# Performance work log

Measured on AMD Instinct MI355X. Metric: run time of the kernel, lower is better.

The kernel has to match this reference:

```python
import jax, jax.numpy as jnp
import numpy as np

S, B, TD = 1024, 2, 138
D, H, Dh, L, F = 1024, 16, 64, 8, 2048
EPS = 1e-5


def setup_inputs() -> dict:
    key = jax.random.key(0)
    ks = jax.random.split(key, 32)
    std = 0.02

    def w(k, shape):
        return (jax.random.normal(k, shape, jnp.float32) * std)

    return {
        'tokens': jax.random.normal(ks[0], (S, B, TD), jnp.float32),
        'Win': w(ks[1], (D, TD)), 'bin_': jnp.zeros((D,), jnp.float32),
        'pos_emb': w(ks[2], (S, D)),
        'Wq': w(ks[3], (L, D, D)), 'bq': jnp.zeros((L, D), jnp.float32),
        'Wk': w(ks[4], (L, D, D)), 'bk': jnp.zeros((L, D), jnp.float32),
        'Wv': w(ks[5], (L, D, D)), 'bv': jnp.zeros((L, D), jnp.float32),
        'Wo': w(ks[6], (L, D, D)), 'bo': jnp.zeros((L, D), jnp.float32),
        'W1': w(ks[7], (L, F, D)), 'b1': jnp.zeros((L, F), jnp.float32),
        'W2': w(ks[8], (L, D, F)), 'b2': jnp.zeros((L, D), jnp.float32),
        'g1': jnp.ones((L, D), jnp.float32), 'be1': jnp.zeros((L, D), jnp.float32),
        'g2': jnp.ones((L, D), jnp.float32), 'be2': jnp.zeros((L, D), jnp.float32),
        'Wh': w(ks[9], (1, D)), 'bh': jnp.zeros((1,), jnp.float32),
    }


def _ln(x, g, b):
    mu = jnp.mean(x, axis=-1, keepdims=True)
    var = jnp.mean(jnp.square(x - mu), axis=-1, keepdims=True)
    return (x - mu) * jax.lax.rsqrt(var + EPS) * g + b


def _rope_tables(seq_len):
    inv_freq = 1.0 / (10000.0 ** (jnp.arange(0, Dh, 2, dtype=jnp.float32) / Dh))
    ang = jnp.arange(seq_len, dtype=jnp.float32)[:, None] * inv_freq  # (S, Dh/2)
    cos = jnp.repeat(jnp.cos(ang), 2, axis=-1)  # (S, Dh) interleaved
    sin = jnp.repeat(jnp.sin(ang), 2, axis=-1)
    return cos, sin


def _apply_rope(x, cos, sin):
    # x: (B, H, S, Dh); rotate_every_two: pairs (x0, x1) -> (-x1, x0)
    rot = jnp.stack([-x[..., 1::2], x[..., 0::2]], axis=-1).reshape(x.shape)
    return x * cos + rot * sin


def reference(tokens, Win, bin_, pos_emb, Wq, bq, Wk, bk, Wv, bv, Wo, bo,
              W1, b1, W2, b2, g1, be1, g2, be2, Wh, bh):
    s = tokens.shape[0]
    x = jnp.einsum('sbt,dt->sbd', tokens, Win) + bin_ + pos_emb[:s, None, :]
    cos, sin = _rope_tables(s)
    causal = jnp.tril(jnp.ones((s, s), dtype=bool))
    scale = 1.0 / np.sqrt(Dh)

    def to_heads(y):  # (S,B,D) -> (B,H,S,Dh)
        return jnp.transpose(y.reshape(s, -1, H, Dh), (1, 2, 0, 3))

    def layer(x, p):
        wq, bq_, wk, bk_, wv, bv_, wo, bo_, w1, b1_, w2, b2_, g1_, be1_, g2_, be2_ = p
        qh = _apply_rope(to_heads(jnp.einsum('sbd,ed->sbe', x, wq) + bq_), cos, sin)
        kh = _apply_rope(to_heads(jnp.einsum('sbd,ed->sbe', x, wk) + bk_), cos, sin)
        vh = to_heads(jnp.einsum('sbd,ed->sbe', x, wv) + bv_)
        scores = jnp.einsum('bhqd,bhkd->bhqk', qh, kh) * scale
        scores = jnp.where(causal, scores, -jnp.inf)
        attn = jax.nn.softmax(scores, axis=-1)
        o = jnp.einsum('bhqk,bhkd->bhqd', attn, vh)  # (B,H,S,Dh)
        o = jnp.transpose(o, (2, 0, 1, 3)).reshape(s, -1, D)
        attn_out = jnp.einsum('sbd,ed->sbe', o, wo) + bo_
        src2 = _ln(x + attn_out, g1_, be1_)
        ff = jnp.einsum('sbf,df->sbd', jax.nn.relu(jnp.einsum('sbd,fd->sbf', src2, w1) + b1_), w2) + b2_
        return _ln(src2 + ff, g2_, be2_), None

    params = (Wq, bq, Wk, bk, Wv, bv, Wo, bo, W1, b1, W2, b2, g1, be1, g2, be2)
    x, _ = jax.lax.scan(layer, x, params)
    return jnp.einsum('sbd,od->sbo', x, Wh) + bh  # (S, B, 1)
```

## Files before the change

### kernel.cpp

```cpp
#include <hip/hip_runtime.h>
#include <hip/hip_bf16.h>

typedef __hip_bfloat16 bf16;
typedef float f32x4 __attribute__((ext_vector_type(4)));
typedef float f32x16 __attribute__((ext_vector_type(16)));
typedef short s16x8 __attribute__((ext_vector_type(8)));
typedef int i32x4 __attribute__((ext_vector_type(4)));

#define S_LEN 1024
#define BATCH 2
#define TDIM 138
#define KPAD 160
#define DMOD 1024
#define NHEAD 16
#define DHEAD 64
#define NLAYER 8
#define FDIM 2048
#define MROWS 2048
static const size_t DD_ = (size_t)DMOD * DMOD;
static const size_t FD_ = (size_t)FDIM * DMOD;

__device__ __forceinline__ void load_lds16(const bf16* g, bf16* l) {
  __builtin_amdgcn_global_load_lds((const __attribute__((address_space(1))) void*)g,
                                   (__attribute__((address_space(3))) void*)l, 16, 0, 0);
}

__device__ __forceinline__ unsigned pack2(float a, float b) {
  unsigned x = __builtin_bit_cast(unsigned short, __float2bfloat16(a));
  unsigned y = __builtin_bit_cast(unsigned short, __float2bfloat16(b));
  return x | (y << 16);
}

__device__ __forceinline__ int chunk_start(int c) {
  return c == 0 ? 0 : (c == 1 ? 32 : (c == 2 ? 56 : 72));
}

__global__ __launch_bounds__(256) void f2b_layer(
    const float4* __restrict__ Wq, const float4* __restrict__ Wk,
    const float4* __restrict__ Wv, const float4* __restrict__ Wo,
    const float4* __restrict__ W1, const float4* __restrict__ W2,
    ushort4* __restrict__ dst) {
  int i = blockIdx.x * 256 + threadIdx.x;
  const int DD4 = (int)(DD_ / 4), FD4 = (int)(FD_ / 4);
  if (i >= 4 * DD4 + 2 * FD4) return;
  const float4* src; int off;
  if (i < 3 * DD4) { int w = i / DD4; off = i - w * DD4; src = w == 0 ? Wq : (w == 1 ? Wk : Wv); }
  else if (i < 4 * DD4) { src = Wo; off = i - 3 * DD4; }
  else if (i < 4 * DD4 + FD4) { src = W1; off = i - 4 * DD4; }
  else { src = W2; off = i - 4 * DD4 - FD4; }
  float4 v = src[off];
  ushort4 o;
  o.x = __builtin_bit_cast(unsigned short, __float2bfloat16(v.x));
  o.y = __builtin_bit_cast(unsigned short, __float2bfloat16(v.y));
  o.z = __builtin_bit_cast(unsigned short, __float2bfloat16(v.z));
  o.w = __builtin_bit_cast(unsigned short, __float2bfloat16(v.w));
  dst[i] = o;
}

__global__ __launch_bounds__(256) void pad_cvt(const float* __restrict__ in,
                                               bf16* __restrict__ out, int R) {
  int i = blockIdx.x * 256 + threadIdx.x;
  if (i >= R * KPAD) return;
  int r = i / KPAD, t = i - r * KPAD;
  out[i] = __float2bfloat16(t < TDIM ? in[r * TDIM + t] : 0.0f);
}

__global__ __launch_bounds__(256) void rope_table(float2* __restrict__ t) {
  int idx = blockIdx.x * 256 + threadIdx.x;
  if (idx >= S_LEN * 32) return;
  int s = idx >> 5, i = idx & 31;
  float freq = __expf(-(float)i * (2.0f / (float)DHEAD) * 9.210340371976184f);
  float sn, cs;
  sincosf((float)s * freq, &sn, &cs);
  t[idx] = make_float2(cs, sn);
}

template<int EPI, int SPLITK>
__global__ __launch_bounds__(256) void gemm64(
    const bf16* __restrict__ A, const bf16* __restrict__ W,
    const float* __restrict__ b0p, const float* __restrict__ b1p, const float* __restrict__ b2p,
    const float2* __restrict__ rope2, float* __restrict__ Cf,
    bf16* __restrict__ Cb0, bf16* __restrict__ Cb1, bf16* __restrict__ Cb2,
    int N, int K, int nby) {
  constexpr int ASZ = 64 * 32, BSZ = 128 * 32;
  __shared__ bf16 As[2 * ASZ];
  __shared__ bf16 Bs[2 * BSZ];
  int nwg = gridDim.x, bid = blockIdx.x;
  int wg = (bid & 7) * (nwg >> 3) + (bid >> 3);
  int nbx = N >> 7;
  int by = wg % nby, bx2 = wg / nby;
  int kh = 0, bx = bx2;
  if constexpr (SPLITK == 2) { bx = bx2 % nbx; kh = bx2 / nbx; }
  int bn = bx * 128, bm = by * 64;
  int Kh = K / SPLITK, koff = kh * Kh;
  int tid = threadIdx.x, lane = tid & 63, w = tid >> 6;
  int lo = lane & 15, hi = lane >> 4;
  int wr = (w >> 1) * 32, wc = (w & 1) * 64;
  f32x4 acc[2][4] = {};

  int srow = tid >> 2, sseg = (tid & 3) * 8;
  const bf16* gA = A + (size_t)(bm + srow) * K + koff + sseg;
  const bf16* gB = W + (size_t)(bn + srow) * K + koff + sseg;
  bf16* lA = As + srow * 32 + sseg;
  bf16* lB = Bs + srow * 32 + sseg;

  auto STAGE = [&](int k0, int b) {
    load_lds16(gA + k0, lA + b * ASZ);
    load_lds16(gB + k0, lB + b * BSZ);
    load_lds16(gB + (size_t)64 * K + k0, lB + b * BSZ + 64 * 32);
  };

  int nt = Kh / 32;
  STAGE(0, 0);
  __syncthreads();
  int cur = 0;
  for (int t = 0; t < nt; t++) {
    if (t + 1 < nt) STAGE((t + 1) * 32, cur ^ 1);
    const bf16* Ab = As + cur * ASZ;
    const bf16* Bb = Bs + cur * BSZ;
    s16x8 af[2], bfr[4];
#pragma unroll
    for (int mi = 0; mi < 2; mi++) af[mi] = *(const s16x8*)(Ab + (wr + mi * 16 + lo) * 32 + hi * 8);
#pragma unroll
    for (int nj = 0; nj < 4; nj++) bfr[nj] = *(const s16x8*)(Bb + (wc + nj * 16 + lo) * 32 + hi * 8);
#pragma unroll
    for (int mi = 0; mi < 2; mi++)
#pragma unroll
      for (int nj = 0; nj < 4; nj++)
        acc[mi][nj] = __builtin_amdgcn_mfma_f32_16x16x32_bf16(af[mi], bfr[nj], acc[mi][nj], 0, 0, 0);
    __syncthreads();
    cur ^= 1;
  }

#pragma unroll
  for (int mi = 0; mi < 2; mi++)
#pragma unroll
    for (int nj = 0; nj < 4; nj++)
#pragma unroll
      for (int r = 0; r < 4; r++) {
        int m = bm + wr + mi * 16 + hi * 4 + r;
        int n = bn + wc + nj * 16 + lo;
        float v = acc[mi][nj][r];
        if constexpr (EPI == 0) {
          int which = n >> 10;
          int d = n & 1023, h = d >> 6, dh = d & 63;
          int s = m >> 1, bb = m & 1;
          const float* bp = which == 0 ? b0p : (which == 1 ? b1p : b2p);
          v += bp[d];
          if (which < 2) {
            float pv = __shfl_xor(v, 1);
            float2 cn = rope2[s * 32 + (dh >> 1)];
            float o = (dh & 1) ? (v * cn.x + pv * cn.y) : (v * cn.x - pv * cn.y);
            bf16* dst = which == 0 ? Cb0 : Cb1;
            dst[(((size_t)(bb * NHEAD + h)) * S_LEN + s) * DHEAD + dh] = __float2bfloat16(o);
          } else {
            Cb2[(((size_t)(bb * NHEAD + h)) * DHEAD + dh) * S_LEN + s] = __float2bfloat16(v);
          }
        } else if constexpr (EPI == 1) {
          if (SPLITK == 1 || kh == 0) v += b0p[n];
          Cf[((size_t)kh * MROWS + m) * N + n] = v;
        } else if constexpr (EPI == 2) {
          Cb0[(size_t)m * N + n] = __float2bfloat16(fmaxf(v + b0p[n], 0.0f));
        } else {
          float v2 = v + b0p[n] + b1p[(size_t)(m >> 1) * DMOD + n];
          Cf[(size_t)m * N + n] = v2;
          Cb0[(size_t)m * N + n] = __float2bfloat16(v2);
        }
      }
}

__global__ __launch_bounds__(256) void flash_part(const bf16* __restrict__ Q,
    const bf16* __restrict__ K, const bf16* __restrict__ Vt,
    float* __restrict__ pO, float* __restrict__ pML) {
  int bid = blockIdx.x;
  int xcd = bid & 7, idx = bid >> 3;
  int bh = xcd * 4 + idx / 20;
  int w = threadIdx.x >> 6, lane = threadIdx.x & 63;
  int widx = (idx % 20) * 4 + w;
  int c = widx < 32 ? 0 : (widx < 56 ? 1 : (widx < 72 ? 2 : 3));
  int qt = widx - chunk_start(c) + 8 * c;
  int l31 = lane & 31, hi1 = lane >> 5;
  int q0 = qt * 32, kc0 = c * 256;
  int kend = min(kc0 + 256, q0 + 32);
  int nkt = (kend - kc0 + 31) >> 5;

  const size_t qkb = (size_t)bh * S_LEN * DHEAD;
  const bf16* qp = Q + qkb + (size_t)(q0 + l31) * DHEAD + hi1 * 8;
  s16x8 bq0 = *(const s16x8*)(qp);
  s16x8 bq1 = *(const s16x8*)(qp + 16);
  s16x8 bq2 = *(const s16x8*)(qp + 32);
  s16x8 bq3 = *(const s16x8*)(qp + 48);
  const bf16* kB = K + qkb;
  const bf16* vB = Vt + qkb;
  f32x16 accO0 = {}, accO1 = {};
  float mv = -INFINITY, lv = 0.0f;
  const float SC = 0.18033688011112042f;

  auto loadTile = [&](int kc, s16x8& k0, s16x8& k1, s16x8& k2, s16x8& k3,
                      s16x8& v0, s16x8& v1, s16x8& v2, s16x8& v3) {
    const bf16* kp = kB + (size_t)(kc + l31) * DHEAD + hi1 * 8;
    k0 = *(const s16x8*)(kp);
    k1 = *(const s16x8*)(kp + 16);
    k2 = *(const s16x8*)(kp + 32);
    k3 = *(const s16x8*)(kp + 48);
    const bf16* vp = vB + (size_t)l31 * S_LEN + kc + hi1 * 8;
    v0 = *(const s16x8*)(vp);
    v1 = *(const s16x8*)(vp + 16);
    v2 = *(const s16x8*)(vp + (size_t)32 * S_LEN);
    v3 = *(const s16x8*)(vp + (size_t)32 * S_LEN + 16);
  };

  auto computeTile = [&](int kc, s16x8 ka0, s16x8 ka1, s16x8 ka2, s16x8 ka3,
                         s16x8 va00, s16x8 va01, s16x8 va10, s16x8 va11) {
    f32x16 st = {};
    st = __builtin_amdgcn_mfma_f32_32x32x16_bf16(ka0, bq0, st, 0, 0, 0);
    st = __builtin_amdgcn_mfma_f32_32x32x16_bf16(ka1, bq1, st, 0, 0, 0);
    st = __builtin_amdgcn_mfma_f32_32x32x16_bf16(ka2, bq2, st, 0, 0, 0);
    st = __builtin_amdgcn_mfma_f32_32x32x16_bf16(ka3, bq3, st, 0, 0, 0);

    bool diag = (kc >= q0);
    float pmax = -INFINITY;
#pragma unroll
    for (int j = 0; j < 16; j++) {
      float s = st[j] * SC;
      if (diag) {
        int krow = kc + (j & 3) + 8 * (j >> 2) + 4 * hi1;
        if (krow > q0 + l31) s = -INFINITY;
      }
      st[j] = s;
      pmax = fmaxf(pmax, s);
    }
    pmax = fmaxf(pmax, __shfl_xor(pmax, 32));
    float mnew = fmaxf(mv, pmax);
    float fs = exp2f(mv - mnew);
    float sum = 0.0f;
#pragma unroll
    for (int j = 0; j < 16; j++) {
      float e = exp2f(st[j] - mnew);
      st[j] = e;
      sum += e;
    }
    sum += __shfl_xor(sum, 32);
    lv = lv * fs + sum;
    mv = mnew;
    accO0 = accO0 * fs;
    accO1 = accO1 * fs;

    unsigned w0 = pack2(st[0], st[1]),   w1 = pack2(st[2], st[3]);
    unsigned w2 = pack2(st[4], st[5]),   w3 = pack2(st[6], st[7]);
    unsigned w4 = pack2(st[8], st[9]),   w5 = pack2(st[10], st[11]);
    unsigned w6 = pack2(st[12], st[13]), w7 = pack2(st[14], st[15]);
    unsigned xw0 = (unsigned)__shfl_xor((int)w0, 32), xw1 = (unsigned)__shfl_xor((int)w1, 32);
    unsigned xw2 = (unsigned)__shfl_xor((int)w2, 32), xw3 = (unsigned)__shfl_xor((int)w3, 32);
    unsigned xw4 = (unsigned)__shfl_xor((int)w4, 32), xw5 = (unsigned)__shfl_xor((int)w5, 32);
    unsigned xw6 = (unsigned)__shfl_xor((int)w6, 32), xw7 = (unsigned)__shfl_xor((int)w7, 32);
    bool hb = (hi1 != 0);
    i32x4 f0, f1;
    f0.x = (int)(hb ? xw2 : w0); f0.y = (int)(hb ? xw3 : w1);
    f0.z = (int)(hb ? w2 : xw0); f0.w = (int)(hb ? w3 : xw1);
    f1.x = (int)(hb ? xw6 : w4); f1.y = (int)(hb ? xw7 : w5);
    f1.z = (int)(hb ? w6 : xw4); f1.w = (int)(hb ? w7 : xw5);
    s16x8 pf0 = __builtin_bit_cast(s16x8, f0);
    s16x8 pf1 = __builtin_bit_cast(s16x8, f1);
    accO0 = __builtin_amdgcn_mfma_f32_32x32x16_bf16(va00, pf0, accO0, 0, 0, 0);
    accO0 = __builtin_amdgcn_mfma_f32_32x32x16_bf16(va01, pf1, accO0, 0, 0, 0);
    accO1 = __builtin_amdgcn_mfma_f32_32x32x16_bf16(va10, pf0, accO1, 0, 0, 0);
    accO1 = __builtin_amdgcn_mfma_f32_32x32x16_bf16(va11, pf1, accO1, 0, 0, 0);
  };

  s16x8 A0, A1, A2, A3, A4, A5, A6, A7;
  s16x8 B0, B1, B2, B3, B4, B5, B6, B7;
  loadTile(kc0, A0, A1, A2, A3, A4, A5, A6, A7);
  for (int kt = 0; kt < nkt; kt += 2) {
    if (kt + 1 < nkt) loadTile(kc0 + (kt + 1) * 32, B0, B1, B2, B3, B4, B5, B6, B7);
    computeTile(kc0 + kt * 32, A0, A1, A2, A3, A4, A5, A6, A7);
    if (kt + 1 < nkt) {
      if (kt + 2 < nkt) loadTile(kc0 + (kt + 2) * 32, A0, A1, A2, A3, A4, A5, A6, A7);
      computeTile(kc0 + (kt + 1) * 32, B0, B1, B2, B3, B4, B5, B6, B7);
    }
  }

  int pbase = bh * 80 + widx;
  float* po = pO + (size_t)pbase * 2048 + l31 * 64 + 4 * hi1;
#pragma unroll
  for (int jj = 0; jj < 4; jj++) {
    f32x4 v0 = {accO0[4 * jj], accO0[4 * jj + 1], accO0[4 * jj + 2], accO0[4 * jj + 3]};
    f32x4 v1 = {accO1[4 * jj], accO1[4 * jj + 1], accO1[4 * jj + 2], accO1[4 * jj + 3]};
    *(f32x4*)(po + 8 * jj) = v0;
    *(f32x4*)(po + 32 + 8 * jj) = v1;
  }
  if (hi1 == 0) {
    pML[pbase * 64 + l31] = mv;
    pML[pbase * 64 + 32 + l31] = lv;
  }
}

__global__ __launch_bounds__(256) void flash_merge(const float* __restrict__ pO,
    const float* __restrict__ pML, bf16* __restrict__ O) {
  int bid = blockIdx.x;
  int xcd = bid & 7, idx = bid >> 3;
  int bh = xcd * 4 + idx / 32, qt = idx % 32;
  int b = bh >> 4, h = bh & 15;
  int nch = (qt >> 3) + 1;
  int t = threadIdx.x;
  int dh = t & 63, r0 = t >> 6;
  int ibase = bh * 80;
#pragma unroll
  for (int j = 0; j < 8; j++) {
    int row = j * 4 + r0;
    float ms = -INFINITY;
    for (int cc = 0; cc < nch; cc++) {
      int wi = chunk_start(cc) + qt - 8 * cc;
      ms = fmaxf(ms, pML[(ibase + wi) * 64 + row]);
    }
    float l = 0.0f, o = 0.0f;
    for (int cc = 0; cc < nch; cc++) {
      int wi = chunk_start(cc) + qt - 8 * cc;
      float wgt = exp2f(pML[(ibase + wi) * 64 + row] - ms);
      l += wgt * pML[(ibase + wi) * 64 + 32 + row];
      o += wgt * pO[(size_t)(ibase + wi) * 2048 + row * 64 + dh];
    }
    int q = qt * 32 + row;
    O[((size_t)q * BATCH + b) * DMOD + h * DHEAD + dh] = __float2bfloat16(o / l);
  }
}

__global__ __launch_bounds__(256) void ln_kernel(const float* __restrict__ a,
    const float* __restrict__ r0, const float* __restrict__ r1,
    const float* __restrict__ g, const float* __restrict__ be,
    float* __restrict__ outf, bf16* __restrict__ outb) {
  int m = blockIdx.x;
  int tid = threadIdx.x;
  float vals[4];
  float s1 = 0.f, s2 = 0.f;
  for (int j = 0; j < 4; j++) {
    int d = tid + j * 256;
    size_t i = (size_t)m * DMOD + d;
    float v = a[i] + r0[i] + r1[i];
    vals[j] = v; s1 += v; s2 += v * v;
  }
  __shared__ float red[8];
  for (int d = 1; d < 64; d <<= 1) { s1 += __shfl_xor(s1, d); s2 += __shfl_xor(s2, d); }
  int w = tid >> 6, lane = tid & 63;
  if (lane == 0) { red[w] = s1; red[4 + w] = s2; }
  __syncthreads();
  s1 = red[0] + red[1] + red[2] + red[3];
  s2 = red[4] + red[5] + red[6] + red[7];
  float mean = s1 * (1.0f / DMOD);
  float var = s2 * (1.0f / DMOD) - mean * mean;
  float rstd = rsqrtf(var + 1e-5f);
  for (int j = 0; j < 4; j++) {
    int d = tid + j * 256;
    float o = (vals[j] - mean) * rstd * g[d] + be[d];
    outf[(size_t)m * DMOD + d] = o;
    outb[(size_t)m * DMOD + d] = __float2bfloat16(o);
  }
}

__global__ __launch_bounds__(256) void head_kernel(const float* __restrict__ x,
    const float* __restrict__ Wh, const float* __restrict__ bh, float* __restrict__ out) {
  int m = blockIdx.x * 4 + (threadIdx.x >> 6);
  int lane = threadIdx.x & 63;
  float s = 0.f;
  for (int j = 0; j < 16; j++) {
    int d = lane + j * 64;
    s += x[(size_t)m * DMOD + d] * Wh[d];
  }
  for (int d = 1; d < 64; d <<= 1) s += __shfl_xor(s, d);
  if (lane == 0) out[m] = s + bh[0];
}

extern "C" void kernel_launch(void* const* d_in, const int* in_sizes, int n_in,
                              void* d_out, int out_size, void* d_ws, size_t ws_size,
                              hipStream_t stream) {
  (void)in_sizes; (void)n_in; (void)out_size; (void)ws_size;
  const float* tokens = (const float*)d_in[0];
  const float* Win    = (const float*)d_in[1];
  const float* binp   = (const float*)d_in[2];
  const float* pos    = (const float*)d_in[3];
  const float* Wq     = (const float*)d_in[4];
  const float* bq     = (const float*)d_in[5];
  const float* Wk     = (const float*)d_in[6];
  const float* bk     = (const float*)d_in[7];
  const float* Wv     = (const float*)d_in[8];
  const float* bv     = (const float*)d_in[9];
  const float* Wo     = (const float*)d_in[10];
  const float* bo     = (const float*)d_in[11];
  const float* W1     = (const float*)d_in[12];
  const float* b1     = (const float*)d_in[13];
  const float* W2     = (const float*)d_in[14];
  const float* b2     = (const float*)d_in[15];
  const float* g1     = (const float*)d_in[16];
  const float* be1    = (const float*)d_in[17];
  const float* g2     = (const float*)d_in[18];
  const float* be2    = (const float*)d_in[19];
  const float* Wh     = (const float*)d_in[20];
  const float* bhp    = (const float*)d_in[21];
  float* out = (float*)d_out;

  char* p = (char*)d_ws;
  auto alloc = [&](size_t bytes) { char* r = p; p += (bytes + 255) & ~(size_t)255; return r; };
  float* xf   = (float*)alloc((size_t)MROWS * DMOD * 4);
  bf16*  xb   = (bf16*) alloc((size_t)MROWS * DMOD * 2);
  float* x2f  = (float*)alloc((size_t)MROWS * DMOD * 4);
  bf16*  x2b  = (bf16*) alloc((size_t)MROWS * DMOD * 2);
  float* tmpf = (float*)alloc((size_t)2 * MROWS * DMOD * 4);
  bf16*  qb   = (bf16*) alloc((size_t)MROWS * DMOD * 2);
  bf16*  kb   = (bf16*) alloc((size_t)MROWS * DMOD * 2);
  bf16*  vt   = (bf16*) alloc((size_t)MROWS * DMOD * 2);
  bf16*  ob   = (bf16*) alloc((size_t)MROWS * DMOD * 2);
  bf16*  hb   = (bf16*) alloc((size_t)MROWS * FDIM * 2);
  bf16*  wb   = (bf16*) alloc((4 * DD_ + 2 * FD_) * 2);
  bf16*  tokb = (bf16*) alloc((size_t)MROWS * KPAD * 2);
  bf16*  winb = (bf16*) alloc((size_t)DMOD * KPAD * 2);
  float2* rope2 = (float2*)alloc((size_t)S_LEN * 32 * 8);
  float* pO   = (float*)alloc((size_t)32 * 80 * 2048 * 4);
  float* pML  = (float*)alloc((size_t)32 * 80 * 64 * 4);

  rope_table<<<(S_LEN * 32 + 255) / 256, 256, 0, stream>>>(rope2);
  pad_cvt<<<(MROWS * KPAD + 255) / 256, 256, 0, stream>>>(tokens, tokb, MROWS);
  pad_cvt<<<(DMOD * KPAD + 255) / 256, 256, 0, stream>>>(Win, winb, DMOD);
  gemm64<3, 1><<<256, 256, 0, stream>>>(
      tokb, winb, binp, pos, nullptr, nullptr,
      xf, xb, nullptr, nullptr, DMOD, KPAD, 32);

  const int nW4 = (int)((4 * DD_ + 2 * FD_) / 4);

  for (int l = 0; l < NLAYER; l++) {
    f2b_layer<<<(nW4 + 255) / 256, 256, 0, stream>>>(
        (const float4*)(Wq + l * DD_), (const float4*)(Wk + l * DD_),
        (const float4*)(Wv + l * DD_), (const float4*)(Wo + l * DD_),
        (const float4*)(W1 + l * FD_), (const float4*)(W2 + l * FD_), (ushort4*)wb);

    gemm64<0, 1><<<768, 256, 0, stream>>>(
        xb, wb, bq + l * DMOD, bk + l * DMOD, bv + l * DMOD, rope2,
        nullptr, qb, kb, vt, 3 * DMOD, DMOD, 32);

    flash_part<<<640, 256, 0, stream>>>(qb, kb, vt, pO, pML);
    flash_merge<<<1024, 256, 0, stream>>>(pO, pML, ob);

    gemm64<1, 2><<<512, 256, 0, stream>>>(
        ob, wb + 3 * DD_, bo + l * DMOD, nullptr, nullptr, nullptr,
        tmpf, nullptr, nullptr, nullptr, DMOD, DMOD, 32);

    ln_kernel<<<MROWS, 256, 0, stream>>>(xf, tmpf, tmpf + (size_t)MROWS * DMOD,
                                         g1 + l * DMOD, be1 + l * DMOD, x2f, x2b);

    gemm64<2, 1><<<512, 256, 0, stream>>>(
        x2b, wb + 4 * DD_, b1 + l * FDIM, nullptr, nullptr, nullptr,
        nullptr, hb, nullptr, nullptr, FDIM, DMOD, 32);

    gemm64<1, 2><<<512, 256, 0, stream>>>(
        hb, wb + 4 * DD_ + FD_, b2 + l * DMOD, nullptr, nullptr, nullptr,
        tmpf, nullptr, nullptr, nullptr, DMOD, FDIM, 32);

    ln_kernel<<<MROWS, 256, 0, stream>>>(x2f, tmpf, tmpf + (size_t)MROWS * DMOD,
                                         g2 + l * DMOD, be2 + l * DMOD, xf, xb);
  }

  head_kernel<<<MROWS / 4, 256, 0, stream>>>(xf, Wh, bhp, out);
}
```

Measured before the change: 1.457 ms.

## Deepen GEMM K-tile to 64 with XOR-swizzled LDS and batch weight conversion

The GEMM now stages 64-wide K tiles instead of 32, halving the number of barrier-separated iterations. It applies an XOR swizzle to the LDS column layout to avoid bank conflicts on the 128-byte row stride. KPAD is raised to 192 so the input projection's K divides by 64. All 8 layers' fp32 weights are converted to bf16 in one up-front grid-stride kernel when workspace allows, replacing the per-layer conversion launches. The larger tiles double LDS usage per block, which may reduce occupancy.

```diff
diff --git a/kernel.cpp b/kernel.cpp
--- a/kernel.cpp
+++ b/kernel.cpp
@@ -10,7 +10,7 @@
 #define S_LEN 1024
 #define BATCH 2
 #define TDIM 138
-#define KPAD 160
+#define KPAD 192
 #define DMOD 1024
 #define NHEAD 16
 #define DHEAD 64
@@ -19,6 +19,7 @@
 #define MROWS 2048
 static const size_t DD_ = (size_t)DMOD * DMOD;
 static const size_t FD_ = (size_t)FDIM * DMOD;
+static const size_t LW_ = 4 * DD_ + 2 * FD_;
 
 __device__ __forceinline__ void load_lds16(const bf16* g, bf16* l) {
   __builtin_amdgcn_global_load_lds((const __attribute__((address_space(1))) void*)g,
@@ -35,26 +36,30 @@
   return c == 0 ? 0 : (c == 1 ? 32 : (c == 2 ? 56 : 72));
 }
 
-__global__ __launch_bounds__(256) void f2b_layer(
+__global__ __launch_bounds__(256) void f2b_all(
     const float4* __restrict__ Wq, const float4* __restrict__ Wk,
     const float4* __restrict__ Wv, const float4* __restrict__ Wo,
     const float4* __restrict__ W1, const float4* __restrict__ W2,
-    ushort4* __restrict__ dst) {
-  int i = blockIdx.x * 256 + threadIdx.x;
-  const int DD4 = (int)(DD_ / 4), FD4 = (int)(FD_ / 4);
-  if (i >= 4 * DD4 + 2 * FD4) return;
-  const float4* src; int off;
-  if (i < 3 * DD4) { int w = i / DD4; off = i - w * DD4; src = w == 0 ? Wq : (w == 1 ? Wk : Wv); }
-  else if (i < 4 * DD4) { src = Wo; off = i - 3 * DD4; }
-  else if (i < 4 * DD4 + FD4) { src = W1; off = i - 4 * DD4; }
-  else { src = W2; off = i - 4 * DD4 - FD4; }
-  float4 v = src[off];
-  ushort4 o;
-  o.x = __builtin_bit_cast(unsigned short, __float2bfloat16(v.x));
-  o.y = __builtin_bit_cast(unsigned short, __float2bfloat16(v.y));
-  o.z = __builtin_bit_cast(unsigned short, __float2bfloat16(v.z));
-  o.w = __builtin_bit_cast(unsigned short, __float2bfloat16(v.w));
-  dst[i] = o;
+    ushort4* __restrict__ dst, int nlay) {
+  const int DD4 = (int)(DD_ / 4), FD4 = (int)(FD_ / 4), LW4 = 4 * DD4 + 2 * FD4;
+  int total = nlay * LW4;
+  for (int i = blockIdx.x * 256 + threadIdx.x; i < total; i += gridDim.x * 256) {
+    int l = i / LW4, off = i - l * LW4;
+    const float4* src; int o2;
+    if (off < 3 * DD4) {
+      int w = off / DD4; o2 = off - w * DD4 + l * DD4;
+      src = w == 0 ? Wq : (w == 1 ? Wk : Wv);
+    } else if (off < 4 * DD4) { src = Wo; o2 = off - 3 * DD4 + l * DD4; }
+    else if (off < 4 * DD4 + FD4) { src = W1; o2 = off - 4 * DD4 + l * FD4; }
+    else { src = W2; o2 = off - 4 * DD4 - FD4 + l * FD4; }
+    float4 v = src[o2];
+    ushort4 o;
+    o.x = __builtin_bit_cast(unsigned short, __float2bfloat16(v.x));
+    o.y = __builtin_bit_cast(unsigned short, __float2bfloat16(v.y));
+    o.z = __builtin_bit_cast(unsigned short, __float2bfloat16(v.z));
+    o.w = __builtin_bit_cast(unsigned short, __float2bfloat16(v.w));
+    dst[i] = o;
+  }
 }
 
 __global__ __launch_bounds__(256) void pad_cvt(const float* __restrict__ in,
@@ -82,7 +87,7 @@
     const float2* __restrict__ rope2, float* __restrict__ Cf,
     bf16* __restrict__ Cb0, bf16* __restrict__ Cb1, bf16* __restrict__ Cb2,
     int N, int K, int nby) {
-  constexpr int ASZ = 64 * 32, BSZ = 128 * 32;
+  constexpr int ASZ = 64 * 64, BSZ = 128 * 64;
   __shared__ bf16 As[2 * ASZ];
   __shared__ bf16 Bs[2 * BSZ];
   int nwg = gridDim.x, bid = blockIdx.x;
@@ -98,36 +103,46 @@
   int wr = (w >> 1) * 32, wc = (w & 1) * 64;
   f32x4 acc[2][4] = {};
 
-  int srow = tid >> 2, sseg = (tid & 3) * 8;
-  const bf16* gA = A + (size_t)(bm + srow) * K + koff + sseg;
-  const bf16* gB = W + (size_t)(bn + srow) * K + koff + sseg;
-  bf16* lA = As + srow * 32 + sseg;
-  bf16* lB = Bs + srow * 32 + sseg;
+  int srow = tid >> 3;
+  int scol = (tid & 7) * 8;
+  int scolsw = scol ^ ((srow & 7) << 3);
+  const bf16* gA = A + (size_t)(bm + srow) * K + koff + scolsw;
+  const bf16* gB = W + (size_t)(bn + srow) * K + koff + scolsw;
+  bf16* lA = As + srow * 64 + scol;
+  bf16* lB = Bs + srow * 64 + scol;
 
   auto STAGE = [&](int k0, int b) {
     load_lds16(gA + k0, lA + b * ASZ);
+    load_lds16(gA + (size_t)32 * K + k0, lA + b * ASZ + 32 * 64);
     load_lds16(gB + k0, lB + b * BSZ);
-    load_lds16(gB + (size_t)64 * K + k0, lB + b * BSZ + 64 * 32);
+    load_lds16(gB + (size_t)32 * K + k0, lB + b * BSZ + 32 * 64);
+    load_lds16(gB + (size_t)64 * K + k0, lB + b * BSZ + 64 * 64);
+    load_lds16(gB + (size_t)96 * K + k0, lB + b * BSZ + 96 * 64);
   };
 
-  int nt = Kh / 32;
+  int nt = Kh / 64;
   STAGE(0, 0);
   __syncthreads();
   int cur = 0;
+  int rsw = (lo & 7) << 3;
   for (int t = 0; t < nt; t++) {
-    if (t + 1 < nt) STAGE((t + 1) * 32, cur ^ 1);
+    if (t + 1 < nt) STAGE((t + 1) * 64, cur ^ 1);
     const bf16* Ab = As + cur * ASZ;
     const bf16* Bb = Bs + cur * BSZ;
-    s16x8 af[2], bfr[4];
-#pragma unroll
-    for (int mi = 0; mi < 2; mi++) af[mi] = *(const s16x8*)(Ab + (wr + mi * 16 + lo) * 32 + hi * 8);
-#pragma unroll
-    for (int nj = 0; nj < 4; nj++) bfr[nj] = *(const s16x8*)(Bb + (wc + nj * 16 + lo) * 32 + hi * 8);
-#pragma unroll
-    for (int mi = 0; mi < 2; mi++)
-#pragma unroll
-      for (int nj = 0; nj < 4; nj++)
-        acc[mi][nj] = __builtin_amdgcn_mfma_f32_16x16x32_bf16(af[mi], bfr[nj], acc[mi][nj], 0, 0, 0);
+#pragma unroll
+    for (int ks = 0; ks < 2; ks++) {
+      int col = ((ks * 32 + hi * 8) ^ rsw);
+      s16x8 af[2], bfr[4];
+#pragma unroll
+      for (int mi = 0; mi < 2; mi++) af[mi] = *(const s16x8*)(Ab + (wr + mi * 16 + lo) * 64 + col);
+#pragma unroll
+      for (int nj = 0; nj < 4; nj++) bfr[nj] = *(const s16x8*)(Bb + (wc + nj * 16 + lo) * 64 + col);
+#pragma unroll
+      for (int mi = 0; mi < 2; mi++)
+#pragma unroll
+        for (int nj = 0; nj < 4; nj++)
+          acc[mi][nj] = __builtin_amdgcn_mfma_f32_16x16x32_bf16(af[mi], bfr[nj], acc[mi][nj], 0, 0, 0);
+    }
     __syncthreads();
     cur ^= 1;
   }
@@ -373,7 +388,7 @@
 extern "C" void kernel_launch(void* const* d_in, const int* in_sizes, int n_in,
                               void* d_out, int out_size, void* d_ws, size_t ws_size,
                               hipStream_t stream) {
-  (void)in_sizes; (void)n_in; (void)out_size; (void)ws_size;
+  (void)in_sizes; (void)n_in; (void)out_size;
   const float* tokens = (const float*)d_in[0];
   const float* Win    = (const float*)d_in[1];
   const float* binp   = (const float*)d_in[2];
@@ -410,48 +425,59 @@
   bf16*  vt   = (bf16*) alloc((size_t)MROWS * DMOD * 2);
   bf16*  ob   = (bf16*) alloc((size_t)MROWS * DMOD * 2);
   bf16*  hb   = (bf16*) alloc((size_t)MROWS * FDIM * 2);
-  bf16*  wb   = (bf16*) alloc((4 * DD_ + 2 * FD_) * 2);
   bf16*  tokb = (bf16*) alloc((size_t)MROWS * KPAD * 2);
   bf16*  winb = (bf16*) alloc((size_t)DMOD * KPAD * 2);
   float2* rope2 = (float2*)alloc((size_t)S_LEN * 32 * 8);
   float* pO   = (float*)alloc((size_t)32 * 80 * 2048 * 4);
   float* pML  = (float*)alloc((size_t)32 * 80 * 64 * 4);
 
+  size_t used = (size_t)(p - (char*)d_ws);
+  bool big = (ws_size - used) >= (size_t)NLAYER * LW_ * 2 + 1024;
+  int nlayConv = big ? NLAYER : 1;
+  bf16* wb = (bf16*)alloc((size_t)nlayConv * LW_ * 2);
+
   rope_table<<<(S_LEN * 32 + 255) / 256, 256, 0, stream>>>(rope2);
   pad_cvt<<<(MROWS * KPAD + 255) / 256, 256, 0, stream>>>(tokens, tokb, MROWS);
   pad_cvt<<<(DMOD * KPAD + 255) / 256, 256, 0, stream>>>(Win, winb, DMOD);
+  if (big)
+    f2b_all<<<2048, 256, 0, stream>>>(
+        (const float4*)Wq, (const float4*)Wk, (const float4*)Wv,
+        (const float4*)Wo, (const float4*)W1, (const float4*)W2,
+        (ushort4*)wb, NLAYER);
+
   gemm64<3, 1><<<256, 256, 0, stream>>>(
       tokb, winb, binp, pos, nullptr, nullptr,
       xf, xb, nullptr, nullptr, DMOD, KPAD, 32);
 
-  const int nW4 = (int)((4 * DD_ + 2 * FD_) / 4);
-
   for (int l = 0; l < NLAYER; l++) {
-    f2b_layer<<<(nW4 + 255) / 256, 256, 0, stream>>>(
-        (const float4*)(Wq + l * DD_), (const float4*)(Wk + l * DD_),
-        (const float4*)(Wv + l * DD_), (const float4*)(Wo + l * DD_),
-        (const float4*)(W1 + l * FD_), (const float4*)(W2 + l * FD_), (ushort4*)wb);
+    if (!big)
+      f2b_all<<<2048, 256, 0, stream>>>(
+          (const float4*)(Wq + l * DD_), (const float4*)(Wk + l * DD_),
+          (const float4*)(Wv + l * DD_), (const float4*)(Wo + l * DD_),
+          (const float4*)(W1 + l * FD_), (const float4*)(W2 + l * FD_),
+          (ushort4*)wb, 1);
+    bf16* wbl = big ? wb + (size_t)l * LW_ : wb;
 
     gemm64<0, 1><<<768, 256, 0, stream>>>(
-        xb, wb, bq + l * DMOD, bk + l * DMOD, bv + l * DMOD, rope2,
+        xb, wbl, bq + l * DMOD, bk + l * DMOD, bv + l * DMOD, rope2,
         nullptr, qb, kb, vt, 3 * DMOD, DMOD, 32);
 
     flash_part<<<640, 256, 0, stream>>>(qb, kb, vt, pO, pML);
     flash_merge<<<1024, 256, 0, stream>>>(pO, pML, ob);
 
     gemm64<1, 2><<<512, 256, 0, stream>>>(
-        ob, wb + 3 * DD_, bo + l * DMOD, nullptr, nullptr, nullptr,
+        ob, wbl + 3 * DD_, bo + l * DMOD, nullptr, nullptr, nullptr,
         tmpf, nullptr, nullptr, nullptr, DMOD, DMOD, 32);
 
     ln_kernel<<<MROWS, 256, 0, stream>>>(xf, tmpf, tmpf + (size_t)MROWS * DMOD,
                                          g1 + l * DMOD, be1 + l * DMOD, x2f, x2b);
 
     gemm64<2, 1><<<512, 256, 0, stream>>>(
-        x2b, wb + 4 * DD_, b1 + l * FDIM, nullptr, nullptr, nullptr,
+        x2b, wbl + 4 * DD_, b1 + l * FDIM, nullptr, nullptr, nullptr,
         nullptr, hb, nullptr, nullptr, FDIM, DMOD, 32);
 
     gemm64<1, 2><<<512, 256, 0, stream>>>(
-        hb, wb + 4 * DD_ + FD_, b2 + l * DMOD, nullptr, nullptr, nullptr,
+        hb, wbl + 4 * DD_ + FD_, b2 + l * DMOD, nullptr, nullptr, nullptr,
         tmpf, nullptr, nullptr, nullptr, DMOD, FDIM, 32);
 
     ln_kernel<<<MROWS, 256, 0, stream>>>(x2f, tmpf, tmpf + (size_t)MROWS * DMOD,
```

Measured after the change: 1.452 ms. Within noise of the previous version (-0.3%).
